# Kernel optimization log

Measured on AMD Instinct MI355X. Metric: run time of the kernel, lower is better.

## Reference

```python
import jax, jax.numpy as jnp
import numpy as np

# pywt db4 decomposition filters (ascending order)
_DEC_LO = np.array([-0.010597401784997278, 0.032883011666982945, 0.030841381835986965,
                    -0.18703481171888114, -0.02798376941698385, 0.6308807679295904,
                    0.7148465705525415, 0.23037781330885523], dtype=np.float32)
_DEC_HI = np.array([-0.23037781330885523, 0.7148465705525415, -0.6308807679295904,
                    -0.02798376941698385, 0.18703481171888114, 0.030841381835986965,
                    0.032883011666982945, -0.010597401784997278], dtype=np.float32)
# lax.conv is correlation; pytorch_wavelets reverses the pywt filters before F.conv1d,
# so the correlation kernel is the reversed decomposition filter.
_KERNEL = jnp.asarray(np.stack([_DEC_LO[::-1], _DEC_HI[::-1]])[:, None, :])  # [2,1,8]
_FLEN = 8
_LEVEL = 3

def _afb1d(x):
    """One analysis level, zero-padding mode of pytorch_wavelets.
    x: [N, 1, S] -> (lo, hi) each [N, 1, (S+7)//2]."""
    S = x.shape[-1]
    outsize = (S + _FLEN - 1) // 2  # pywt.dwt_coeff_len, mode='zero'
    p = 2 * (outsize - 1) - S + _FLEN
    if p % 2 == 1:
        x = jnp.pad(x, ((0, 0), (0, 0), (0, 1)))
    lohi = jax.lax.conv_general_dilated(
        x, _KERNEL, window_strides=(2,), padding=[(p // 2, p // 2)],
        dimension_numbers=('NCH', 'OIH', 'NCH'))
    return lohi[:, 0:1, :], lohi[:, 1:2, :]


def setup_inputs() -> dict:
    key = jax.random.key(0)
    x = jax.random.normal(key, (8, 4096, 128), dtype=jnp.float32)
    return {"x": x}


def reference(x):
    B, S, F = x.shape
    lo = x.transpose(0, 2, 1).reshape(B * F, 1, S)  # channel-wise DWT
    details_c = []
    for _ in range(_LEVEL):
        lo, hi = _afb1d(lo)
        details_c.append(hi)

    def place(c):
        # zero-pad coeffs back to full seq_len, layout [B, S, F]
        c = c.reshape(B, F, -1).transpose(0, 2, 1)
        out = jnp.zeros((B, S, F), dtype=x.dtype)
        return out.at[:, :c.shape[1], :].set(c)

    approx = place(lo)
    details = [place(h) for h in details_c]
    high_freq = details[0] + details[1] + details[2]
    low_freq = approx
    # stack: [approx, d1, d2, d3, high_freq, low_freq] -> [6, B, S, F]
    return jnp.stack([approx, details[0], details[1], details[2], high_freq, low_freq])
```

## Files before the change

### kernel.cpp

```cpp
#include <hip/hip_runtime.h>

__device__ __constant__ float LOF[8] = {
    -0.010597401784997278f,  0.032883011666982945f,  0.030841381835986965f,
    -0.18703481171888114f,  -0.02798376941698385f,   0.6308807679295904f,
     0.7148465705525415f,    0.23037781330885523f};
__device__ __constant__ float HIF[8] = {
    -0.23037781330885523f,   0.7148465705525415f,   -0.6308807679295904f,
    -0.02798376941698385f,   0.18703481171888114f,   0.030841381835986965f,
     0.032883011666982945f, -0.010597401784997278f};

__global__ void dwt_level_kernel(const float4* __restrict__ in,
                                 float4* __restrict__ out_lo,
                                 float4* __restrict__ out_hi,
                                 int Sin, int Sout, int in_bs, int lo_bs, int hi_bs) {
    int idx = blockIdx.x * 256 + threadIdx.x;
    int total = 8 * Sout * 32;
    if (idx >= total) return;
    int f    = idx & 31;
    int rest = idx >> 5;
    int t    = rest % Sout;
    int b    = rest / Sout;
    const float4* ib = in + b * in_bs + f;
    float4 lo = {0.f, 0.f, 0.f, 0.f};
    float4 hi = {0.f, 0.f, 0.f, 0.f};
    int s0 = 2 * t + 1;
#pragma unroll
    for (int j = 0; j < 8; ++j) {
        int s = s0 - j;
        if (s >= 0 && s < Sin) {
            float4 v = ib[s * 32];
            float cl = LOF[j], ch = HIF[j];
            lo.x = fmaf(cl, v.x, lo.x); lo.y = fmaf(cl, v.y, lo.y);
            lo.z = fmaf(cl, v.z, lo.z); lo.w = fmaf(cl, v.w, lo.w);
            hi.x = fmaf(ch, v.x, hi.x); hi.y = fmaf(ch, v.y, hi.y);
            hi.z = fmaf(ch, v.z, hi.z); hi.w = fmaf(ch, v.w, hi.w);
        }
    }
    out_lo[b * lo_bs + t * 32 + f] = lo;
    out_hi[b * hi_bs + t * 32 + f] = hi;
}

__global__ void assemble_kernel(float4* __restrict__ out) {
    int idx = blockIdx.x * 256 + threadIdx.x;
    int f    = idx & 31;
    int rest = idx >> 5;
    int s    = rest & 4095;
    long base = (long)rest * 32 + f;
    const long CH = 8L * 4096 * 32;
    float4 z = {0.f, 0.f, 0.f, 0.f};
    float4 v0, v1, v2, v3;
    if (s < 518)  { v0 = out[base]; }          else { v0 = z; out[base] = z; }
    if (s < 2051) { v1 = out[CH + base]; }     else { v1 = z; out[CH + base] = z; }
    if (s < 1029) { v2 = out[2 * CH + base]; } else { v2 = z; out[2 * CH + base] = z; }
    if (s < 518)  { v3 = out[3 * CH + base]; } else { v3 = z; out[3 * CH + base] = z; }
    float4 hsum;
    hsum.x = v1.x + v2.x + v3.x;
    hsum.y = v1.y + v2.y + v3.y;
    hsum.z = v1.z + v2.z + v3.z;
    hsum.w = v1.w + v2.w + v3.w;
    out[4 * CH + base] = hsum;
    out[5 * CH + base] = v0;
}

extern "C" void kernel_launch(void* const* d_in, const int* in_sizes, int n_in,
                              void* d_out, int out_size, void* d_ws, size_t ws_size,
                              hipStream_t stream) {
    const float4* x   = (const float4*)d_in[0];
    float4*       out = (float4*)d_out;
    float4* lo1 = (float4*)d_ws;
    float4* lo2 = lo1 + 8 * 2051 * 32;

    const long CH = 8L * 4096 * 32;
    float4* c0 = out;
    float4* c1 = out + CH;
    float4* c2 = out + 2 * CH;
    float4* c3 = out + 3 * CH;

    {
        int total = 8 * 2051 * 32;
        dwt_level_kernel<<<(total + 255) / 256, 256, 0, stream>>>(
            x, lo1, c1, 4096, 2051, 4096 * 32, 2051 * 32, 4096 * 32);
    }
    {
        int total = 8 * 1029 * 32;
        dwt_level_kernel<<<(total + 255) / 256, 256, 0, stream>>>(
            lo1, lo2, c2, 2051, 1029, 2051 * 32, 1029 * 32, 4096 * 32);
    }
    {
        int total = 8 * 518 * 32;
        dwt_level_kernel<<<(total + 255) / 256, 256, 0, stream>>>(
            lo2, c0, c3, 1029, 518, 1029 * 32, 4096 * 32, 4096 * 32);
    }
    assemble_kernel<<<4096, 256, 0, stream>>>(out);
}
```

Measured before the change: 131.0 us.

## Fuse three DWT levels and assembly into one kernel via composed filters

Replaces the three per-level DWT kernels and the assembly kernel with a single kernel. Levels 2 and 3 are computed directly from the input using composed filters (22-tap and 50-tap) built at compile time, so no intermediate low-pass buffers are needed. Each output element is written exactly once, zeros included, which removes the read-modify-write assembly pass and three extra launches. The cost is more redundant FMAs and input reads per level-3 thread (50 taps), and composing the filters in double then rounding to float changes the numerics slightly. The block-index swizzle spreads the heavier level-3 rows across the grid.

```diff
diff --git a/kernel.cpp b/kernel.cpp
--- a/kernel.cpp
+++ b/kernel.cpp
@@ -1,65 +1,103 @@
 #include <hip/hip_runtime.h>
 
-__device__ __constant__ float LOF[8] = {
-    -0.010597401784997278f,  0.032883011666982945f,  0.030841381835986965f,
-    -0.18703481171888114f,  -0.02798376941698385f,   0.6308807679295904f,
-     0.7148465705525415f,    0.23037781330885523f};
-__device__ __constant__ float HIF[8] = {
-    -0.23037781330885523f,   0.7148465705525415f,   -0.6308807679295904f,
-    -0.02798376941698385f,   0.18703481171888114f,   0.030841381835986965f,
-     0.032883011666982945f, -0.010597401784997278f};
 
-__global__ void dwt_level_kernel(const float4* __restrict__ in,
-                                 float4* __restrict__ out_lo,
-                                 float4* __restrict__ out_hi,
-                                 int Sin, int Sout, int in_bs, int lo_bs, int hi_bs) {
-    int idx = blockIdx.x * 256 + threadIdx.x;
-    int total = 8 * Sout * 32;
-    if (idx >= total) return;
-    int f    = idx & 31;
-    int rest = idx >> 5;
-    int t    = rest % Sout;
-    int b    = rest / Sout;
-    const float4* ib = in + b * in_bs + f;
-    float4 lo = {0.f, 0.f, 0.f, 0.f};
-    float4 hi = {0.f, 0.f, 0.f, 0.f};
-    int s0 = 2 * t + 1;
+struct Weights {
+    float w1h[8];
+    float w2h[22];
+    float w3h[50];
+    float w3l[50];
+};
+
+constexpr Weights make_weights() {
+    constexpr double LO[8] = {
+        -0.010597401784997278,  0.032883011666982945,  0.030841381835986965,
+        -0.18703481171888114,  -0.02798376941698385,   0.6308807679295904,
+         0.7148465705525415,    0.23037781330885523};
+    constexpr double HI[8] = {
+        -0.23037781330885523,   0.7148465705525415,   -0.6308807679295904,
+        -0.02798376941698385,   0.18703481171888114,   0.030841381835986965,
+         0.032883011666982945, -0.010597401784997278};
+    double a2h[22] = {}, a3h[50] = {}, a3l[50] = {};
+    for (int j = 0; j < 8; ++j)
+        for (int k = 0; k < 8; ++k)
+            a2h[2 * j + k] += HI[j] * LO[k];
+    for (int j = 0; j < 8; ++j)
+        for (int k = 0; k < 8; ++k)
+            for (int l = 0; l < 8; ++l) {
+                a3h[4 * j + 2 * k + l] += HI[j] * LO[k] * LO[l];
+                a3l[4 * j + 2 * k + l] += LO[j] * LO[k] * LO[l];
+            }
+    Weights W = {};
+    for (int i = 0; i < 8; ++i)  W.w1h[i] = (float)HI[i];
+    for (int i = 0; i < 22; ++i) W.w2h[i] = (float)a2h[i];
+    for (int i = 0; i < 50; ++i) { W.w3h[i] = (float)a3h[i]; W.w3l[i] = (float)a3l[i]; }
+    return W;
+}
+
+__device__ __constant__ Weights CW = make_weights();
+
+__device__ __forceinline__ void fma4(float4& a, float c, const float4& v) {
+    a.x = fmaf(c, v.x, a.x);
+    a.y = fmaf(c, v.y, a.y);
+    a.z = fmaf(c, v.z, a.z);
+    a.w = fmaf(c, v.w, a.w);
+}
+
+__global__ void __launch_bounds__(256) wavelet_fused_kernel(
+        const float4* __restrict__ x, float4* __restrict__ out) {
+    int c     = blockIdx.x;
+    int chunk = ((c & 7) << 6) | (c >> 3);
+    int s     = chunk * 8 + (threadIdx.x >> 5);
+    int f     = threadIdx.x & 31;
+    int b     = blockIdx.y;
+
+    const float4* xb = x + (long)b * 4096 * 32 + f;
+    const float4 z = {0.f, 0.f, 0.f, 0.f};
+    float4 h1 = z, h2 = z, h3 = z, l3 = z;
+
+    if (s < 2051) {
+        int r0 = 2 * s + 1;
 #pragma unroll
-    for (int j = 0; j < 8; ++j) {
-        int s = s0 - j;
-        if (s >= 0 && s < Sin) {
-            float4 v = ib[s * 32];
-            float cl = LOF[j], ch = HIF[j];
-            lo.x = fmaf(cl, v.x, lo.x); lo.y = fmaf(cl, v.y, lo.y);
-            lo.z = fmaf(cl, v.z, lo.z); lo.w = fmaf(cl, v.w, lo.w);
-            hi.x = fmaf(ch, v.x, hi.x); hi.y = fmaf(ch, v.y, hi.y);
-            hi.z = fmaf(ch, v.z, hi.z); hi.w = fmaf(ch, v.w, hi.w);
+        for (int j = 0; j < 8; ++j) {
+            int r = r0 - j;
+            float4 v = ((unsigned)r < 4096u) ? xb[r * 32] : z;
+            fma4(h1, CW.w1h[j], v);
         }
     }
-    out_lo[b * lo_bs + t * 32 + f] = lo;
-    out_hi[b * hi_bs + t * 32 + f] = hi;
-}
+    if (s < 1029) {
+        int r0 = 4 * s + 3;
+#pragma unroll
+        for (int m = 0; m < 22; ++m) {
+            int r = r0 - m;
+            float4 v = ((unsigned)r < 4096u) ? xb[r * 32] : z;
+            fma4(h2, CW.w2h[m], v);
+        }
+    }
+    if (s < 518) {
+        int r0 = 8 * s + 7;
+#pragma unroll
+        for (int m = 0; m < 50; ++m) {
+            int r = r0 - m;
+            float4 v = ((unsigned)r < 4096u) ? xb[r * 32] : z;
+            fma4(h3, CW.w3h[m], v);
+            fma4(l3, CW.w3l[m], v);
+        }
+    }
 
-__global__ void assemble_kernel(float4* __restrict__ out) {
-    int idx = blockIdx.x * 256 + threadIdx.x;
-    int f    = idx & 31;
-    int rest = idx >> 5;
-    int s    = rest & 4095;
-    long base = (long)rest * 32 + f;
+    float4 hs;
+    hs.x = h1.x + h2.x + h3.x;
+    hs.y = h1.y + h2.y + h3.y;
+    hs.z = h1.z + h2.z + h3.z;
+    hs.w = h1.w + h2.w + h3.w;
+
     const long CH = 8L * 4096 * 32;
-    float4 z = {0.f, 0.f, 0.f, 0.f};
-    float4 v0, v1, v2, v3;
-    if (s < 518)  { v0 = out[base]; }          else { v0 = z; out[base] = z; }
-    if (s < 2051) { v1 = out[CH + base]; }     else { v1 = z; out[CH + base] = z; }
-    if (s < 1029) { v2 = out[2 * CH + base]; } else { v2 = z; out[2 * CH + base] = z; }
-    if (s < 518)  { v3 = out[3 * CH + base]; } else { v3 = z; out[3 * CH + base] = z; }
-    float4 hsum;
-    hsum.x = v1.x + v2.x + v3.x;
-    hsum.y = v1.y + v2.y + v3.y;
-    hsum.z = v1.z + v2.z + v3.z;
-    hsum.w = v1.w + v2.w + v3.w;
-    out[4 * CH + base] = hsum;
-    out[5 * CH + base] = v0;
+    long base = ((long)b * 4096 + s) * 32 + f;
+    out[base]          = l3;
+    out[CH + base]     = h1;
+    out[2 * CH + base] = h2;
+    out[3 * CH + base] = h3;
+    out[4 * CH + base] = hs;
+    out[5 * CH + base] = l3;
 }
 
 extern "C" void kernel_launch(void* const* d_in, const int* in_sizes, int n_in,
@@ -67,29 +105,6 @@
                               hipStream_t stream) {
     const float4* x   = (const float4*)d_in[0];
     float4*       out = (float4*)d_out;
-    float4* lo1 = (float4*)d_ws;
-    float4* lo2 = lo1 + 8 * 2051 * 32;
-
-    const long CH = 8L * 4096 * 32;
-    float4* c0 = out;
-    float4* c1 = out + CH;
-    float4* c2 = out + 2 * CH;
-    float4* c3 = out + 3 * CH;
-
-    {
-        int total = 8 * 2051 * 32;
-        dwt_level_kernel<<<(total + 255) / 256, 256, 0, stream>>>(
-            x, lo1, c1, 4096, 2051, 4096 * 32, 2051 * 32, 4096 * 32);
-    }
-    {
-        int total = 8 * 1029 * 32;
-        dwt_level_kernel<<<(total + 255) / 256, 256, 0, stream>>>(
-            lo1, lo2, c2, 2051, 1029, 2051 * 32, 1029 * 32, 4096 * 32);
-    }
-    {
-        int total = 8 * 518 * 32;
-        dwt_level_kernel<<<(total + 255) / 256, 256, 0, stream>>>(
-            lo2, c0, c3, 1029, 518, 1029 * 32, 4096 * 32, 4096 * 32);
-    }
-    assemble_kernel<<<4096, 256, 0, stream>>>(out);
+    dim3 grid(512, 8);
+    wavelet_fused_kernel<<<grid, 256, 0, stream>>>(x, out);
 }
```

Measured after the change: 379.3 us. 2.89x slower.
